# Kernel optimization log

Measured on AMD Instinct MI355X. Metric: run time of the kernel, lower is better.

The kernel has to match this reference:

```python
import jax, jax.numpy as jnp
import numpy as np

HEAD_DIM = 128
NUM_Q_HEADS = 16
NUM_KV_HEADS = 8
EPS = 1e-6


def _rope_tables(seq_len, head_dim, base=10000.0):
    inv_freq = 1.0 / (base ** (np.arange(0, head_dim, 2, dtype=np.float32) / head_dim))
    t = np.arange(seq_len, dtype=np.float32)
    freqs = np.outer(t, inv_freq)                      # [S, hd/2]
    emb = np.concatenate([freqs, freqs], axis=-1)      # [S, hd]
    return jnp.asarray(np.cos(emb)), jnp.asarray(np.sin(emb))


def setup_inputs() -> dict:
    key = jax.random.key(0)
    k1, k2, k3 = jax.random.split(key, 3)
    B, S, D = 2, 2048, 2048
    qo_dim = NUM_Q_HEADS * HEAD_DIM
    kv_dim = NUM_KV_HEADS * HEAD_DIM
    x = jax.random.normal(k1, (B, S, D), dtype=jnp.float32)
    w_qkv = jax.random.normal(k2, (qo_dim + 2 * kv_dim, D), dtype=jnp.float32) * 0.02
    w_o = jax.random.normal(k3, (D, qo_dim), dtype=jnp.float32) * 0.02
    pos_cos, pos_sin = _rope_tables(S, HEAD_DIM)
    return {
        "x": x,
        "pos_cos": pos_cos,
        "pos_sin": pos_sin,
        "w_qkv": w_qkv,
        "w_o": w_o,
        "q_norm_w": jnp.ones((HEAD_DIM,), dtype=jnp.float32),
        "k_norm_w": jnp.ones((HEAD_DIM,), dtype=jnp.float32),
    }


def _rms_norm(h, w):
    # per-head RMSNorm over last dim (head_dim)
    var = jnp.mean(jnp.square(h), axis=-1, keepdims=True)
    return h * jax.lax.rsqrt(var + EPS) * w


def _rotate_half(h):
    h1, h2 = jnp.split(h, 2, axis=-1)
    return jnp.concatenate([-h2, h1], axis=-1)


def _apply_rope(h, cos, sin):
    # h: [B, S, H, hd]; cos/sin: [S, hd]
    c = cos[None, :, None, :]
    s = sin[None, :, None, :]
    return h * c + _rotate_half(h) * s


def reference(x, pos_cos, pos_sin, w_qkv, w_o, q_norm_w, k_norm_w):
    B, S, D = x.shape
    hd = HEAD_DIM
    qkv = jnp.einsum("bsd,ed->bse", x, w_qkv).reshape(B, S, -1, hd)
    q = qkv[:, :, :NUM_Q_HEADS]                                   # [B,S,Hq,hd]
    k = qkv[:, :, NUM_Q_HEADS:NUM_Q_HEADS + NUM_KV_HEADS]         # [B,S,Hk,hd]
    v = qkv[:, :, NUM_Q_HEADS + NUM_KV_HEADS:]                    # [B,S,Hk,hd]

    q = _apply_rope(_rms_norm(q, q_norm_w), pos_cos, pos_sin)
    k = _apply_rope(_rms_norm(k, k_norm_w), pos_cos, pos_sin)

    # GQA: expand kv heads to match query heads
    rep = NUM_Q_HEADS // NUM_KV_HEADS
    k = jnp.repeat(k, rep, axis=2)
    v = jnp.repeat(v, rep, axis=2)

    scale = 1.0 / jnp.sqrt(jnp.float32(hd))
    scores = jnp.einsum("bqhd,bkhd->bhqk", q, k) * scale          # [B,H,S,S]
    causal = jnp.tril(jnp.ones((S, S), dtype=bool))
    scores = jnp.where(causal[None, None], scores, jnp.finfo(scores.dtype).min)
    attn = jax.nn.softmax(scores, axis=-1)
    out = jnp.einsum("bhqk,bkhd->bqhd", attn, v)                  # [B,S,H,hd]
    out = out.reshape(B, S, NUM_Q_HEADS * hd)
    return jnp.einsum("bse,de->bsd", out, w_o)
```

## Files before the change

### kernel.cpp

```cpp
#include <hip/hip_runtime.h>
#include <hip/hip_bf16.h>
#include <stdint.h>

#define HD 128
#define NQH 16
#define NKVH 8
#define SEQ 2048
#define DMODEL 2048
#define BATCH 2

typedef __attribute__((ext_vector_type(8))) short bf16x8;
typedef __attribute__((ext_vector_type(4))) float f32x4;
typedef __attribute__((ext_vector_type(16))) float f32x16;

__device__ __forceinline__ ushort f2bf(float f){
  union { float f; uint32_t u; } v; v.f = f;
  uint32_t u = v.u;
  return (ushort)((u + 0x7FFFu + ((u >> 16) & 1u)) >> 16);
}
__device__ __forceinline__ float bf2f(ushort h){
  union { uint32_t u; float f; } v; v.u = ((uint32_t)h) << 16; return v.f;
}
__device__ __forceinline__ void gload16(const void* g, void* l){
  __builtin_amdgcn_global_load_lds((const __attribute__((address_space(1))) void*)g,
                                   (__attribute__((address_space(3))) void*)l, 16, 0, 0);
}
__device__ __forceinline__ unsigned int cvtpk(float lo, float hi){
  unsigned int r;
  asm("v_cvt_pk_bf16_f32 %0, %1, %2" : "=v"(r) : "v"(lo), "v"(hi));
  return r;
}

__global__ void cvtbf(const float* __restrict__ in, ushort* __restrict__ out, int n4){
  int i = blockIdx.x * 256 + threadIdx.x;
  if (i < n4){
    float4 v = ((const float4*)in)[i];
    ushort4 o;
    o.x = f2bf(v.x); o.y = f2bf(v.y); o.z = f2bf(v.z); o.w = f2bf(v.w);
    ((ushort4*)out)[i] = o;
  }
}

template<int OUTF32>
__global__ __launch_bounds__(256) void gemm_bt(const ushort* __restrict__ A,
                                               const ushort* __restrict__ B,
                                               void* __restrict__ C,
                                               int M, int N, int K){
  __shared__ __align__(16) ushort lA[128*64];
  __shared__ __align__(16) ushort lB[128*64];
  const int tid = threadIdx.x;
  const int l = tid & 63, w = tid >> 6;
  const int m0 = blockIdx.y * 128, n0 = blockIdx.x * 128;
  const int wr = (w >> 1) * 64, wc = (w & 1) * 64;
  f32x4 acc[4][4];
  #pragma unroll
  for (int m=0;m<4;m++)
    #pragma unroll
    for (int n=0;n<4;n++) acc[m][n] = f32x4{0.f,0.f,0.f,0.f};

  const int srow = l >> 3;
  const int scol = ((l & 7) ^ srow) << 3;
  const ushort* gA = A + (size_t)(m0 + w*32 + srow) * K + scol;
  const ushort* gB = B + (size_t)(n0 + w*32 + srow) * K + scol;
  ushort* lAw = &lA[(w*32) * 64];
  ushort* lBw = &lB[(w*32) * 64];

  for (int kt = 0; kt < K; kt += 64){
    __syncthreads();
    #pragma unroll
    for (int j=0;j<4;j++){
      gload16(gA + kt + (size_t)(j*8)*K, lAw + j*8*64);
      gload16(gB + kt + (size_t)(j*8)*K, lBw + j*8*64);
    }
    __syncthreads();
    #pragma unroll
    for (int kk=0; kk<2; kk++){
      bf16x8 af[4], bb[4];
      #pragma unroll
      for (int m=0;m<4;m++){
        int row = wr + m*16 + (l & 15);
        int slot = (kk*4 + (l >> 4)) ^ (row & 7);
        af[m] = *(const bf16x8*)&lA[row*64 + slot*8];
      }
      #pragma unroll
      for (int n=0;n<4;n++){
        int row = wc + n*16 + (l & 15);
        int slot = (kk*4 + (l >> 4)) ^ (row & 7);
        bb[n] = *(const bf16x8*)&lB[row*64 + slot*8];
      }
      #pragma unroll
      for (int m=0;m<4;m++)
        #pragma unroll
        for (int n=0;n<4;n++)
          acc[m][n] = __builtin_amdgcn_mfma_f32_16x16x32_bf16(af[m], bb[n], acc[m][n], 0,0,0);
    }
  }
  #pragma unroll
  for (int m=0;m<4;m++)
    #pragma unroll
    for (int n=0;n<4;n++)
      #pragma unroll
      for (int r=0;r<4;r++){
        size_t row = (size_t)(m0 + wr + m*16 + (l>>4)*4 + r);
        size_t col = (size_t)(n0 + wc + n*16 + (l & 15));
        float v = acc[m][n][r];
        if (OUTF32) ((float*)C)[row*N + col] = v;
        else        ((ushort*)C)[row*N + col] = f2bf(v);
      }
}

__global__ __launch_bounds__(512, 1) void gemm256_bt(const ushort* __restrict__ A,
                                                     const ushort* __restrict__ B,
                                                     ushort* __restrict__ C,
                                                     int M, int N, int K){
  __shared__ __align__(16) ushort lA[2][256*64];
  __shared__ __align__(16) ushort lB[2][256*64];
  const int tid = threadIdx.x;
  const int l = tid & 63, w = tid >> 6;
  const int wm = w >> 2, wn = w & 3;
  const int m0 = blockIdx.y * 256, n0 = blockIdx.x * 256;
  const int NT = K >> 6;

  const int srow = w*8 + (l >> 3);
  const int scol = ((l & 7) ^ (l >> 3)) << 3;

  f32x4 acc[8][4];
  #pragma unroll
  for (int m=0;m<8;m++)
    #pragma unroll
    for (int n=0;n<4;n++) acc[m][n] = f32x4{0.f,0.f,0.f,0.f};

  auto stgA = [&](int t, int h){
    const int bi = t & 1;
    #pragma unroll
    for (int j=0;j<2;j++)
      gload16(A + (size_t)(m0 + h*128 + j*64 + srow)*K + t*64 + scol,
              &lA[bi][(h*128 + j*64 + w*8)*64]);
  };
  auto stgB = [&](int t, int h){
    const int bi = t & 1;
    #pragma unroll
    for (int j=0;j<2;j++)
      gload16(B + (size_t)(n0 + h*128 + j*64 + srow)*K + t*64 + scol,
              &lB[bi][(h*128 + j*64 + w*8)*64]);
  };

  stgA(0,0); stgA(0,1); stgB(0,0); stgB(0,1);
  stgA(1,0); stgB(1,0); stgB(1,1);
  asm volatile("s_waitcnt vmcnt(6)" ::: "memory");
  __builtin_amdgcn_s_barrier();

  for (int t=0; t<NT; t++){
    const int bi = t & 1;
    bf16x8 bfr[4][2];
    #pragma unroll
    for (int q=0; q<4; q++){
      bf16x8 af[2][2];
      #pragma unroll
      for (int mi2=0; mi2<2; mi2++)
        #pragma unroll
        for (int ks=0; ks<2; ks++){
          int row = wm*128 + (q*2 + mi2)*16 + (l & 15);
          int slot = (ks*4 + (l >> 4)) ^ (l & 7);
          af[mi2][ks] = *(const bf16x8*)&lA[bi][row*64 + slot*8];
        }
      if (q == 0){
        #pragma unroll
        for (int ni=0; ni<4; ni++)
          #pragma unroll
          for (int ks=0; ks<2; ks++){
            int row = wn*64 + ni*16 + (l & 15);
            int slot = (ks*4 + (l >> 4)) ^ (l & 7);
            bfr[ni][ks] = *(const bf16x8*)&lB[bi][row*64 + slot*8];
          }
      }
      if (q == 0 && t+1 < NT) stgA(t+1, 1);
      if (q == 1 && t+2 < NT) stgB(t+2, 0);
      if (q == 2 && t+2 < NT) stgB(t+2, 1);
      __builtin_amdgcn_s_barrier();
      asm volatile("s_waitcnt lgkmcnt(0)" ::: "memory");
      if (q == 3 && t+2 < NT) stgA(t+2, 0);
      __builtin_amdgcn_s_setprio(1);
      #pragma unroll
      for (int mi2=0; mi2<2; mi2++)
        #pragma unroll
        for (int ni=0; ni<4; ni++)
          #pragma unroll
          for (int ks=0; ks<2; ks++)
            acc[q*2+mi2][ni] = __builtin_amdgcn_mfma_f32_16x16x32_bf16(
                af[mi2][ks], bfr[ni][ks], acc[q*2+mi2][ni], 0,0,0);
      __builtin_amdgcn_s_setprio(0);
      if (q == 3){
        if (t < NT-2) { asm volatile("s_waitcnt vmcnt(6)" ::: "memory"); }
        else          { asm volatile("s_waitcnt vmcnt(0)" ::: "memory"); }
      }
      __builtin_amdgcn_s_barrier();
    }
  }

  #pragma unroll
  for (int mi=0; mi<8; mi++)
    #pragma unroll
    for (int ni=0; ni<4; ni++)
      #pragma unroll
      for (int r=0; r<4; r++){
        size_t row = (size_t)(m0 + wm*128 + mi*16 + (l>>4)*4 + r);
        size_t col = (size_t)(n0 + wn*64 + ni*16 + (l & 15));
        C[row*N + col] = f2bf(acc[mi][ni][r]);
      }
}

__global__ __launch_bounds__(256) void norm_rope(const ushort* __restrict__ qkv,
                                                 const float* __restrict__ cosT,
                                                 const float* __restrict__ sinT,
                                                 const float* __restrict__ qw,
                                                 const float* __restrict__ kw,
                                                 ushort* __restrict__ Qo,
                                                 ushort* __restrict__ Ko){
  int gw = (blockIdx.x * 256 + threadIdx.x) >> 6;
  int l = threadIdx.x & 63;
  int head = gw % 24;
  int bs = gw / 24;
  int s = bs & (SEQ-1);
  int b = bs >> 11;
  ushort2 hv = *(const ushort2*)(qkv + (size_t)bs*(2*DMODEL) + head*HD + l*2);
  float h0 = bf2f(hv.x), h1 = bf2f(hv.y);
  float ss = h0*h0 + h1*h1;
  #pragma unroll
  for (int m=1; m<64; m<<=1) ss += __shfl_xor(ss, m);
  float rinv = rsqrtf(ss * (1.0f/128.0f) + 1e-6f);
  const float* wp = (head < NQH) ? qw : kw;
  float w0 = wp[l*2], w1 = wp[l*2+1];
  float n0 = h0 * rinv * w0, n1 = h1 * rinv * w1;
  float p0 = __shfl_xor(n0, 32), p1 = __shfl_xor(n1, 32);
  float r0 = (l < 32) ? -p0 : p0;
  float r1 = (l < 32) ? -p1 : p1;
  float c0 = cosT[s*HD + l*2], c1 = cosT[s*HD + l*2 + 1];
  float s0 = sinT[s*HD + l*2], s1 = sinT[s*HD + l*2 + 1];
  float sc = (head < NQH) ? 0.12751656062f : 1.0f;
  ushort2 o;
  o.x = f2bf((n0*c0 + r0*s0) * sc);
  o.y = f2bf((n1*c1 + r1*s1) * sc);
  if (head < NQH)
    *(ushort2*)(Qo + ((size_t)((b*NQH + head)*SEQ) + s)*HD + l*2) = o;
  else
    *(ushort2*)(Ko + ((size_t)((b*NKVH + (head-NQH))*SEQ) + s)*HD + l*2) = o;
}

__global__ __launch_bounds__(256) void vtrans(const ushort* __restrict__ qkv, ushort* __restrict__ vt){
  __shared__ __align__(16) ushort t[64][136];
  int bid = blockIdx.x;
  int st = bid & 31, kh = (bid >> 5) & 7, b = bid >> 8;
  int s0 = st * 64;
  int tid = threadIdx.x;
  #pragma unroll
  for (int it=0; it<4; it++){
    int row = (tid >> 4) + it*16;
    int c = tid & 15;
    uint4 v = *(const uint4*)&qkv[((size_t)(b*SEQ + s0 + row))*(2*DMODEL) + (NQH+NKVH+kh)*HD + c*8];
    *(uint4*)&t[row][c*8] = v;
  }
  __syncthreads();
  #pragma unroll
  for (int it=0; it<4; it++){
    int g = it*256 + tid;
    int d = g >> 3, c = g & 7;
    ushort tmp[8] __attribute__((aligned(16)));
    #pragma unroll
    for (int j=0;j<8;j++) tmp[j] = t[c*8+j][d];
    *(uint4*)&vt[((size_t)((b*NKVH+kh)*HD + d))*SEQ + s0 + c*8] = *(uint4*)tmp;
  }
}

__global__ __launch_bounds__(256, 2) void attn_fwd(const ushort* __restrict__ Q,
                                                   const ushort* __restrict__ Kb,
                                                   const ushort* __restrict__ Vt,
                                                   ushort* __restrict__ O){
  __shared__ __align__(16) ushort lK[2][64*128];
  __shared__ __align__(16) ushort lV[2][128*64];
  const int l = threadIdx.x & 63, w = threadIdx.x >> 6;
  const int wq = w >> 1, wkv = w & 1;
  const int hl = l >> 5, q32 = l & 31;
  const int e = blockIdx.x, head = blockIdx.y, b = blockIdx.z;
  const int kh = head >> 1;

  const ushort* kg = Kb + (size_t)((b*NKVH + kh)*SEQ) * HD;
  const ushort* vg = Vt + (size_t)((b*NKVH + kh)*HD) * SEQ;

  auto STAGE = [&](int t, int bi){
    const int kv0 = t*64;
    #pragma unroll
    for (int j=0;j<4;j++){
      int krow = kv0 + w*16 + j*4 + (l>>4);
      gload16(kg + (size_t)krow*HD + (((l&15) ^ (krow&15))<<3),
              &lK[bi][(w*16 + j*4)*128]);
      int vrow = w*32 + j*8 + (l>>3);
      gload16(vg + (size_t)vrow*SEQ + kv0 + (((l&7) ^ (l>>3))<<3),
              &lV[bi][(w*32 + j*8)*64]);
    }
  };

  auto run_tile = [&](int qt){
    const int qb = qt*64 + wq*32;
    const ushort* qp = Q + ((size_t)((b*NQH + head)*SEQ) + qb + q32) * HD + hl*8;
    bf16x8 qf[8];
    #pragma unroll
    for (int ks=0; ks<8; ks++) qf[ks] = *(const bf16x8*)(qp + ks*16);

    float mrun = -1e30f, lrun = 0.f;
    f32x16 acc[4];
    #pragma unroll
    for (int dt=0;dt<4;dt++)
      #pragma unroll
      for (int r=0;r<16;r++) acc[dt][r] = 0.f;

    STAGE(0, 0);
    __syncthreads();

    for (int t=0; t<=qt; t++){
      if (t < qt) STAGE(t+1, (t+1)&1);
      const int bi = t & 1;
      const bool skip = (t==qt) && (wq==0) && (wkv==1);
      if (!skip){
        f32x16 s;
        #pragma unroll
        for (int r=0;r<16;r++) s[r] = 0.f;
        const int rowT = wkv*32 + q32;
        #pragma unroll
        for (int ks=0; ks<8; ks++){
          int slot = (ks*2 + hl) ^ (rowT & 15);
          bf16x8 kf = *(const bf16x8*)&lK[bi][rowT*128 + slot*8];
          s = __builtin_amdgcn_mfma_f32_32x32x16_bf16(kf, qf[ks], s, 0,0,0);
        }
        if (t==qt && wq==wkv){
          const int qg = qb + q32;
          #pragma unroll
          for (int r=0;r<16;r++){
            int kvg = t*64 + wkv*32 + (r&3) + 8*(r>>2) + 4*hl;
            s[r] = (kvg > qg) ? -1e30f : s[r];
          }
        }
        float t0 = fmaxf(fmaxf(s[0],s[1]),fmaxf(s[2],s[3]));
        float t1 = fmaxf(fmaxf(s[4],s[5]),fmaxf(s[6],s[7]));
        float t2 = fmaxf(fmaxf(s[8],s[9]),fmaxf(s[10],s[11]));
        float t3 = fmaxf(fmaxf(s[12],s[13]),fmaxf(s[14],s[15]));
        float tmax = fmaxf(fmaxf(t0,t1),fmaxf(t2,t3));
        tmax = fmaxf(tmax, __shfl_xor(tmax, 32));
        if (!__all(tmax <= mrun)){
          float mnew = fmaxf(mrun, tmax);
          float corr = __builtin_amdgcn_exp2f(mrun - mnew);
          mrun = mnew; lrun *= corr;
          #pragma unroll
          for (int r=0;r<16;r++){
            int qr = (r&3) + 8*(r>>2) + 4*hl;
            float cr = __shfl(corr, qr);
            acc[0][r]*=cr; acc[1][r]*=cr; acc[2][r]*=cr; acc[3][r]*=cr;
          }
        }
        #pragma unroll
        for (int r=0;r<16;r++) s[r] = __builtin_amdgcn_exp2f(s[r] - mrun);
        float r0s = (s[0]+s[1])+(s[2]+s[3]);
        float r1s = (s[4]+s[5])+(s[6]+s[7]);
        float r2s = (s[8]+s[9])+(s[10]+s[11]);
        float r3s = (s[12]+s[13])+(s[14]+s[15]);
        float rs = (r0s+r1s)+(r2s+r3s);
        rs += __shfl_xor(rs, 32);
        lrun += rs;
        #pragma unroll
        for (int ks2=0; ks2<2; ks2++){
          unsigned int A = cvtpk(s[8*ks2+0], s[8*ks2+1]);
          unsigned int B = cvtpk(s[8*ks2+2], s[8*ks2+3]);
          unsigned int C = cvtpk(s[8*ks2+4], s[8*ks2+5]);
          unsigned int D = cvtpk(s[8*ks2+6], s[8*ks2+7]);
          auto sw0 = __builtin_amdgcn_permlane32_swap(A, C, false, false);
          auto sw1 = __builtin_amdgcn_permlane32_swap(B, D, false, false);
          union { unsigned int u[4]; bf16x8 v; } pw;
          pw.u[0]=sw0[0]; pw.u[1]=sw1[0]; pw.u[2]=sw0[1]; pw.u[3]=sw1[1];
          #pragma unroll
          for (int dt=0; dt<4; dt++){
            int d = dt*32 + q32;
            int slot = (wkv*4 + ks2*2 + hl) ^ (d & 7);
            bf16x8 vf = *(const bf16x8*)&lV[bi][d*64 + slot*8];
            acc[dt] = __builtin_amdgcn_mfma_f32_32x32x16_bf16(pw.v, vf, acc[dt], 0,0,0);
          }
        }
      }
      __syncthreads();
    }

    float* mergeO = (float*)(&lK[0][0]) + wq*4096;
    float* mergeML = (float*)(&lV[0][0]);
    if (wkv == 1){
      #pragma unroll
      for (int dt=0; dt<4; dt++)
        #pragma unroll
        for (int rg=0; rg<4; rg++){
          f32x4 o = { acc[dt][rg*4+0], acc[dt][rg*4+1], acc[dt][rg*4+2], acc[dt][rg*4+3] };
          *(f32x4*)&mergeO[(dt*4+rg)*256 + l*4] = o;
        }
      if (l < 32){
        mergeML[wq*64 + l] = mrun;
        mergeML[wq*64 + 32 + l] = lrun;
      }
    }
    __syncthreads();
    if (wkv == 0){
      float m1 = mergeML[wq*64 + q32];
      float l1 = mergeML[wq*64 + 32 + q32];
      float mf = fmaxf(mrun, m1);
      float c0 = __builtin_amdgcn_exp2f(mrun - mf);
      float c1 = __builtin_amdgcn_exp2f(m1 - mf);
      float lt = lrun*c0 + l1*c1;
      float linv = 1.0f / lt;
      float f0 = c0 * linv, f1 = c1 * linv;
      float g0a[16], g1a[16];
      #pragma unroll
      for (int r=0;r<16;r++){
        int qr = (r&3) + 8*(r>>2) + 4*hl;
        g0a[r] = __shfl(f0, qr);
        g1a[r] = __shfl(f1, qr);
      }
      #pragma unroll
      for (int dt=0; dt<4; dt++)
        #pragma unroll
        for (int rg=0; rg<4; rg++){
          f32x4 o1 = *(const f32x4*)&mergeO[(dt*4+rg)*256 + l*4];
          #pragma unroll
          for (int j=0;j<4;j++){
            int r = rg*4 + j;
            int qr = (r&3) + 8*(r>>2) + 4*hl;
            float val = acc[dt][r]*g0a[r] + o1[j]*g1a[r];
            int orow = qt*64 + wq*32 + qr;
            O[((size_t)(b*SEQ) + orow)*DMODEL + head*HD + dt*32 + q32] = f2bf(val);
          }
        }
    }
    __syncthreads();
  };

  run_tile(e);
  run_tile(31 - e);
}

extern "C" void kernel_launch(void* const* d_in, const int* in_sizes, int n_in,
                              void* d_out, int out_size, void* d_ws, size_t ws_size,
                              hipStream_t stream){
  const float* x    = (const float*)d_in[0];
  const float* pcos = (const float*)d_in[1];
  const float* psin = (const float*)d_in[2];
  const float* wqkv = (const float*)d_in[3];
  const float* wo   = (const float*)d_in[4];
  const float* qnw  = (const float*)d_in[5];
  const float* knw  = (const float*)d_in[6];
  char* ws = (char*)d_ws;

  ushort* xb    = (ushort*)(ws + 0);
  ushort* wqkvb = (ushort*)(ws + 16777216);
  ushort* wob   = (ushort*)(ws + 33554432);
  ushort* qkv   = (ushort*)(ws + 41943040);
  ushort* qbuf  = (ushort*)(ws + 75497472);
  ushort* kbuf  = (ushort*)(ws + 92274688);
  ushort* vtb   = (ushort*)(ws + 100663296);
  ushort* aout  = (ushort*)(ws + 0);

  cvtbf<<<8192, 256, 0, stream>>>(x,    xb,    2097152);
  cvtbf<<<8192, 256, 0, stream>>>(wqkv, wqkvb, 2097152);
  cvtbf<<<4096, 256, 0, stream>>>(wo,   wob,   1048576);

  gemm256_bt<<<dim3(16,16), 512, 0, stream>>>(xb, wqkvb, qkv, 4096, 4096, 2048);

  norm_rope<<<24576, 256, 0, stream>>>(qkv, pcos, psin, qnw, knw, qbuf, kbuf);
  vtrans<<<512, 256, 0, stream>>>(qkv, vtb);

  attn_fwd<<<dim3(16,16,2), 256, 0, stream>>>(qbuf, kbuf, vtb, aout);

  gemm_bt<1><<<dim3(16,32), 256, 0, stream>>>(aout, wob, d_out, 4096, 2048, 2048);
}
```

Measured before the change: 224.1 us.

## Restructure attention: one q-tile per block, single V buffer, finer-grained waits

Each attention block now handles a single query tile, launched longest-first across a 1D grid of 1024 blocks. Previously each block processed a paired short and long tile to balance causal work. The V LDS buffer drops from double to single buffering so three blocks can share a CU. K for the next tile and V for the current tile are issued together, and explicit vmcnt waits let QK^T and softmax overlap the V load. MFMA phases are bracketed with s_setprio, and more barriers are added per iteration, which may cost some synchronisation overhead.

```diff
diff --git a/kernel.cpp b/kernel.cpp
--- a/kernel.cpp
+++ b/kernel.cpp
@@ -272,174 +272,192 @@
   }
 }
 
-__global__ __launch_bounds__(256, 2) void attn_fwd(const ushort* __restrict__ Q,
+__global__ __launch_bounds__(256, 3) void attn_fwd(const ushort* __restrict__ Q,
                                                    const ushort* __restrict__ Kb,
                                                    const ushort* __restrict__ Vt,
                                                    ushort* __restrict__ O){
   __shared__ __align__(16) ushort lK[2][64*128];
-  __shared__ __align__(16) ushort lV[2][128*64];
+  __shared__ __align__(16) ushort lV[128*64];
   const int l = threadIdx.x & 63, w = threadIdx.x >> 6;
   const int wq = w >> 1, wkv = w & 1;
   const int hl = l >> 5, q32 = l & 31;
-  const int e = blockIdx.x, head = blockIdx.y, b = blockIdx.z;
+  const int bid = blockIdx.x;
+  const int qt = 31 - (bid >> 5);
+  const int bh = bid & 31;
+  const int head = bh & 15, b = bh >> 4;
   const int kh = head >> 1;
 
   const ushort* kg = Kb + (size_t)((b*NKVH + kh)*SEQ) * HD;
   const ushort* vg = Vt + (size_t)((b*NKVH + kh)*HD) * SEQ;
 
-  auto STAGE = [&](int t, int bi){
+  auto STAGE_K = [&](int t, int bi){
     const int kv0 = t*64;
     #pragma unroll
     for (int j=0;j<4;j++){
       int krow = kv0 + w*16 + j*4 + (l>>4);
       gload16(kg + (size_t)krow*HD + (((l&15) ^ (krow&15))<<3),
               &lK[bi][(w*16 + j*4)*128]);
+    }
+  };
+  auto STAGE_V = [&](int t){
+    const int kv0 = t*64;
+    #pragma unroll
+    for (int j=0;j<4;j++){
       int vrow = w*32 + j*8 + (l>>3);
       gload16(vg + (size_t)vrow*SEQ + kv0 + (((l&7) ^ (l>>3))<<3),
-              &lV[bi][(w*32 + j*8)*64]);
+              &lV[(w*32 + j*8)*64]);
     }
   };
 
-  auto run_tile = [&](int qt){
-    const int qb = qt*64 + wq*32;
-    const ushort* qp = Q + ((size_t)((b*NQH + head)*SEQ) + qb + q32) * HD + hl*8;
-    bf16x8 qf[8];
-    #pragma unroll
-    for (int ks=0; ks<8; ks++) qf[ks] = *(const bf16x8*)(qp + ks*16);
-
-    float mrun = -1e30f, lrun = 0.f;
-    f32x16 acc[4];
-    #pragma unroll
-    for (int dt=0;dt<4;dt++)
-      #pragma unroll
-      for (int r=0;r<16;r++) acc[dt][r] = 0.f;
-
-    STAGE(0, 0);
-    __syncthreads();
-
-    for (int t=0; t<=qt; t++){
-      if (t < qt) STAGE(t+1, (t+1)&1);
-      const int bi = t & 1;
-      const bool skip = (t==qt) && (wq==0) && (wkv==1);
-      if (!skip){
-        f32x16 s;
-        #pragma unroll
-        for (int r=0;r<16;r++) s[r] = 0.f;
-        const int rowT = wkv*32 + q32;
-        #pragma unroll
-        for (int ks=0; ks<8; ks++){
-          int slot = (ks*2 + hl) ^ (rowT & 15);
-          bf16x8 kf = *(const bf16x8*)&lK[bi][rowT*128 + slot*8];
-          s = __builtin_amdgcn_mfma_f32_32x32x16_bf16(kf, qf[ks], s, 0,0,0);
+  const int qb = qt*64 + wq*32;
+  const ushort* qp = Q + ((size_t)((b*NQH + head)*SEQ) + qb + q32) * HD + hl*8;
+  bf16x8 qf[8];
+  #pragma unroll
+  for (int ks=0; ks<8; ks++) qf[ks] = *(const bf16x8*)(qp + ks*16);
+
+  float mrun = -1e30f, lrun = 0.f;
+  f32x16 acc[4];
+  #pragma unroll
+  for (int dt=0;dt<4;dt++)
+    #pragma unroll
+    for (int r=0;r<16;r++) acc[dt][r] = 0.f;
+
+  STAGE_K(0, 0);
+
+  for (int t=0; t<=qt; t++){
+    const int bi = t & 1;
+    STAGE_V(t);
+    STAGE_K(t < qt ? t+1 : qt, bi^1);
+    asm volatile("s_waitcnt vmcnt(8)" ::: "memory");
+    __builtin_amdgcn_s_barrier();
+
+    const bool skip = (t==qt) && (wq==0) && (wkv==1);
+    f32x16 s;
+    if (!skip){
+      #pragma unroll
+      for (int r=0;r<16;r++) s[r] = 0.f;
+      const int rowT = wkv*32 + q32;
+      __builtin_amdgcn_s_setprio(1);
+      #pragma unroll
+      for (int ks=0; ks<8; ks++){
+        int slot = (ks*2 + hl) ^ (rowT & 15);
+        bf16x8 kf = *(const bf16x8*)&lK[bi][rowT*128 + slot*8];
+        s = __builtin_amdgcn_mfma_f32_32x32x16_bf16(kf, qf[ks], s, 0,0,0);
+      }
+      __builtin_amdgcn_s_setprio(0);
+      if (t==qt && wq==wkv){
+        const int qg = qb + q32;
+        #pragma unroll
+        for (int r=0;r<16;r++){
+          int kvg = t*64 + wkv*32 + (r&3) + 8*(r>>2) + 4*hl;
+          s[r] = (kvg > qg) ? -1e30f : s[r];
         }
-        if (t==qt && wq==wkv){
-          const int qg = qb + q32;
-          #pragma unroll
-          for (int r=0;r<16;r++){
-            int kvg = t*64 + wkv*32 + (r&3) + 8*(r>>2) + 4*hl;
-            s[r] = (kvg > qg) ? -1e30f : s[r];
-          }
+      }
+      float t0 = fmaxf(fmaxf(s[0],s[1]),fmaxf(s[2],s[3]));
+      float t1 = fmaxf(fmaxf(s[4],s[5]),fmaxf(s[6],s[7]));
+      float t2 = fmaxf(fmaxf(s[8],s[9]),fmaxf(s[10],s[11]));
+      float t3 = fmaxf(fmaxf(s[12],s[13]),fmaxf(s[14],s[15]));
+      float tmax = fmaxf(fmaxf(t0,t1),fmaxf(t2,t3));
+      tmax = fmaxf(tmax, __shfl_xor(tmax, 32));
+      if (!__all(tmax <= mrun)){
+        float mnew = fmaxf(mrun, tmax);
+        float corr = __builtin_amdgcn_exp2f(mrun - mnew);
+        mrun = mnew; lrun *= corr;
+        #pragma unroll
+        for (int r=0;r<16;r++){
+          int qr = (r&3) + 8*(r>>2) + 4*hl;
+          float cr = __shfl(corr, qr);
+          acc[0][r]*=cr; acc[1][r]*=cr; acc[2][r]*=cr; acc[3][r]*=cr;
         }
-        float t0 = fmaxf(fmaxf(s[0],s[1]),fmaxf(s[2],s[3]));
-        float t1 = fmaxf(fmaxf(s[4],s[5]),fmaxf(s[6],s[7]));
-        float t2 = fmaxf(fmaxf(s[8],s[9]),fmaxf(s[10],s[11]));
-        float t3 = fmaxf(fmaxf(s[12],s[13]),fmaxf(s[14],s[15]));
-        float tmax = fmaxf(fmaxf(t0,t1),fmaxf(t2,t3));
-        tmax = fmaxf(tmax, __shfl_xor(tmax, 32));
-        if (!__all(tmax <= mrun)){
-          float mnew = fmaxf(mrun, tmax);
-          float corr = __builtin_amdgcn_exp2f(mrun - mnew);
-          mrun = mnew; lrun *= corr;
-          #pragma unroll
-          for (int r=0;r<16;r++){
-            int qr = (r&3) + 8*(r>>2) + 4*hl;
-            float cr = __shfl(corr, qr);
-            acc[0][r]*=cr; acc[1][r]*=cr; acc[2][r]*=cr; acc[3][r]*=cr;
-          }
+      }
+      #pragma unroll
+      for (int r=0;r<16;r++) s[r] = __builtin_amdgcn_exp2f(s[r] - mrun);
+      float r0s = (s[0]+s[1])+(s[2]+s[3]);
+      float r1s = (s[4]+s[5])+(s[6]+s[7]);
+      float r2s = (s[8]+s[9])+(s[10]+s[11]);
+      float r3s = (s[12]+s[13])+(s[14]+s[15]);
+      float rs = (r0s+r1s)+(r2s+r3s);
+      rs += __shfl_xor(rs, 32);
+      lrun += rs;
+    }
+    asm volatile("s_waitcnt vmcnt(4)" ::: "memory");
+    __builtin_amdgcn_s_barrier();
+    if (!skip){
+      __builtin_amdgcn_s_setprio(1);
+      #pragma unroll
+      for (int ks2=0; ks2<2; ks2++){
+        unsigned int A = cvtpk(s[8*ks2+0], s[8*ks2+1]);
+        unsigned int B = cvtpk(s[8*ks2+2], s[8*ks2+3]);
+        unsigned int C = cvtpk(s[8*ks2+4], s[8*ks2+5]);
+        unsigned int D = cvtpk(s[8*ks2+6], s[8*ks2+7]);
+        auto sw0 = __builtin_amdgcn_permlane32_swap(A, C, false, false);
+        auto sw1 = __builtin_amdgcn_permlane32_swap(B, D, false, false);
+        union { unsigned int u[4]; bf16x8 v; } pw;
+        pw.u[0]=sw0[0]; pw.u[1]=sw1[0]; pw.u[2]=sw0[1]; pw.u[3]=sw1[1];
+        #pragma unroll
+        for (int dt=0; dt<4; dt++){
+          int d = dt*32 + q32;
+          int slot = (wkv*4 + ks2*2 + hl) ^ (d & 7);
+          bf16x8 vf = *(const bf16x8*)&lV[d*64 + slot*8];
+          acc[dt] = __builtin_amdgcn_mfma_f32_32x32x16_bf16(pw.v, vf, acc[dt], 0,0,0);
         }
-        #pragma unroll
-        for (int r=0;r<16;r++) s[r] = __builtin_amdgcn_exp2f(s[r] - mrun);
-        float r0s = (s[0]+s[1])+(s[2]+s[3]);
-        float r1s = (s[4]+s[5])+(s[6]+s[7]);
-        float r2s = (s[8]+s[9])+(s[10]+s[11]);
-        float r3s = (s[12]+s[13])+(s[14]+s[15]);
-        float rs = (r0s+r1s)+(r2s+r3s);
-        rs += __shfl_xor(rs, 32);
-        lrun += rs;
-        #pragma unroll
-        for (int ks2=0; ks2<2; ks2++){
-          unsigned int A = cvtpk(s[8*ks2+0], s[8*ks2+1]);
-          unsigned int B = cvtpk(s[8*ks2+2], s[8*ks2+3]);
-          unsigned int C = cvtpk(s[8*ks2+4], s[8*ks2+5]);
-          unsigned int D = cvtpk(s[8*ks2+6], s[8*ks2+7]);
-          auto sw0 = __builtin_amdgcn_permlane32_swap(A, C, false, false);
-          auto sw1 = __builtin_amdgcn_permlane32_swap(B, D, false, false);
-          union { unsigned int u[4]; bf16x8 v; } pw;
-          pw.u[0]=sw0[0]; pw.u[1]=sw1[0]; pw.u[2]=sw0[1]; pw.u[3]=sw1[1];
-          #pragma unroll
-          for (int dt=0; dt<4; dt++){
-            int d = dt*32 + q32;
-            int slot = (wkv*4 + ks2*2 + hl) ^ (d & 7);
-            bf16x8 vf = *(const bf16x8*)&lV[bi][d*64 + slot*8];
-            acc[dt] = __builtin_amdgcn_mfma_f32_32x32x16_bf16(pw.v, vf, acc[dt], 0,0,0);
-          }
+      }
+      __builtin_amdgcn_s_setprio(0);
+    }
+    asm volatile("s_waitcnt lgkmcnt(0)" ::: "memory");
+    __builtin_amdgcn_s_barrier();
+  }
+
+  asm volatile("s_waitcnt vmcnt(0)" ::: "memory");
+  __builtin_amdgcn_s_barrier();
+
+  float* mergeO = (float*)(&lK[0][0]) + wq*4096;
+  float* mergeML = (float*)(&lV[0]);
+  if (wkv == 1){
+    #pragma unroll
+    for (int dt=0; dt<4; dt++)
+      #pragma unroll
+      for (int rg=0; rg<4; rg++){
+        f32x4 o = { acc[dt][rg*4+0], acc[dt][rg*4+1], acc[dt][rg*4+2], acc[dt][rg*4+3] };
+        *(f32x4*)&mergeO[(dt*4+rg)*256 + l*4] = o;
+      }
+    if (l < 32){
+      mergeML[wq*64 + l] = mrun;
+      mergeML[wq*64 + 32 + l] = lrun;
+    }
+  }
+  __syncthreads();
+  if (wkv == 0){
+    float m1 = mergeML[wq*64 + q32];
+    float l1 = mergeML[wq*64 + 32 + q32];
+    float mf = fmaxf(mrun, m1);
+    float c0 = __builtin_amdgcn_exp2f(mrun - mf);
+    float c1 = __builtin_amdgcn_exp2f(m1 - mf);
+    float lt = lrun*c0 + l1*c1;
+    float linv = 1.0f / lt;
+    float f0 = c0 * linv, f1 = c1 * linv;
+    float g0a[16], g1a[16];
+    #pragma unroll
+    for (int r=0;r<16;r++){
+      int qr = (r&3) + 8*(r>>2) + 4*hl;
+      g0a[r] = __shfl(f0, qr);
+      g1a[r] = __shfl(f1, qr);
+    }
+    #pragma unroll
+    for (int dt=0; dt<4; dt++)
+      #pragma unroll
+      for (int rg=0; rg<4; rg++){
+        f32x4 o1 = *(const f32x4*)&mergeO[(dt*4+rg)*256 + l*4];
+        #pragma unroll
+        for (int j=0;j<4;j++){
+          int r = rg*4 + j;
+          int qr = (r&3) + 8*(r>>2) + 4*hl;
+          float val = acc[dt][r]*g0a[r] + o1[j]*g1a[r];
+          int orow = qt*64 + wq*32 + qr;
+          O[((size_t)(b*SEQ) + orow)*DMODEL + head*HD + dt*32 + q32] = f2bf(val);
         }
       }
-      __syncthreads();
-    }
-
-    float* mergeO = (float*)(&lK[0][0]) + wq*4096;
-    float* mergeML = (float*)(&lV[0][0]);
-    if (wkv == 1){
-      #pragma unroll
-      for (int dt=0; dt<4; dt++)
-        #pragma unroll
-        for (int rg=0; rg<4; rg++){
-          f32x4 o = { acc[dt][rg*4+0], acc[dt][rg*4+1], acc[dt][rg*4+2], acc[dt][rg*4+3] };
-          *(f32x4*)&mergeO[(dt*4+rg)*256 + l*4] = o;
-        }
-      if (l < 32){
-        mergeML[wq*64 + l] = mrun;
-        mergeML[wq*64 + 32 + l] = lrun;
-      }
-    }
-    __syncthreads();
-    if (wkv == 0){
-      float m1 = mergeML[wq*64 + q32];
-      float l1 = mergeML[wq*64 + 32 + q32];
-      float mf = fmaxf(mrun, m1);
-      float c0 = __builtin_amdgcn_exp2f(mrun - mf);
-      float c1 = __builtin_amdgcn_exp2f(m1 - mf);
-      float lt = lrun*c0 + l1*c1;
-      float linv = 1.0f / lt;
-      float f0 = c0 * linv, f1 = c1 * linv;
-      float g0a[16], g1a[16];
-      #pragma unroll
-      for (int r=0;r<16;r++){
-        int qr = (r&3) + 8*(r>>2) + 4*hl;
-        g0a[r] = __shfl(f0, qr);
-        g1a[r] = __shfl(f1, qr);
-      }
-      #pragma unroll
-      for (int dt=0; dt<4; dt++)
-        #pragma unroll
-        for (int rg=0; rg<4; rg++){
-          f32x4 o1 = *(const f32x4*)&mergeO[(dt*4+rg)*256 + l*4];
-          #pragma unroll
-          for (int j=0;j<4;j++){
-            int r = rg*4 + j;
-            int qr = (r&3) + 8*(r>>2) + 4*hl;
-            float val = acc[dt][r]*g0a[r] + o1[j]*g1a[r];
-            int orow = qt*64 + wq*32 + qr;
-            O[((size_t)(b*SEQ) + orow)*DMODEL + head*HD + dt*32 + q32] = f2bf(val);
-          }
-        }
-    }
-    __syncthreads();
-  };
-
-  run_tile(e);
-  run_tile(31 - e);
+  }
 }
 
 extern "C" void kernel_launch(void* const* d_in, const int* in_sizes, int n_in,
@@ -472,7 +490,7 @@
   norm_rope<<<24576, 256, 0, stream>>>(qkv, pcos, psin, qnw, knw, qbuf, kbuf);
   vtrans<<<512, 256, 0, stream>>>(qkv, vtb);
 
-  attn_fwd<<<dim3(16,16,2), 256, 0, stream>>>(qbuf, kbuf, vtb, aout);
+  attn_fwd<<<dim3(1024), 256, 0, stream>>>(qbuf, kbuf, vtb, aout);
 
   gemm_bt<1><<<dim3(16,32), 256, 0, stream>>>(aout, wob, d_out, 4096, 2048, 2048);
 }
```

After: 228.2 us. Within noise of the previous version (+1.8%).

## Replace output projection GEMM with pipelined 256x128 double-buffered kernel

Applied to the files above, without the earlier changes.

Swaps the simple 128x128 single-buffered output-projection GEMM for a 512-thread 256x128 tile kernel. It double-buffers LDS with async global-to-LDS loads staged across sub-iterations and raises MFMA priority. The aim is to hide load latency and improve data reuse per block. It uses more LDS and registers per block, so occupancy drops to one block per CU.

```diff
diff --git a/kernel.cpp b/kernel.cpp
--- a/kernel.cpp
+++ b/kernel.cpp
@@ -39,74 +39,6 @@
     o.x = f2bf(v.x); o.y = f2bf(v.y); o.z = f2bf(v.z); o.w = f2bf(v.w);
     ((ushort4*)out)[i] = o;
   }
-}
-
-template<int OUTF32>
-__global__ __launch_bounds__(256) void gemm_bt(const ushort* __restrict__ A,
-                                               const ushort* __restrict__ B,
-                                               void* __restrict__ C,
-                                               int M, int N, int K){
-  __shared__ __align__(16) ushort lA[128*64];
-  __shared__ __align__(16) ushort lB[128*64];
-  const int tid = threadIdx.x;
-  const int l = tid & 63, w = tid >> 6;
-  const int m0 = blockIdx.y * 128, n0 = blockIdx.x * 128;
-  const int wr = (w >> 1) * 64, wc = (w & 1) * 64;
-  f32x4 acc[4][4];
-  #pragma unroll
-  for (int m=0;m<4;m++)
-    #pragma unroll
-    for (int n=0;n<4;n++) acc[m][n] = f32x4{0.f,0.f,0.f,0.f};
-
-  const int srow = l >> 3;
-  const int scol = ((l & 7) ^ srow) << 3;
-  const ushort* gA = A + (size_t)(m0 + w*32 + srow) * K + scol;
-  const ushort* gB = B + (size_t)(n0 + w*32 + srow) * K + scol;
-  ushort* lAw = &lA[(w*32) * 64];
-  ushort* lBw = &lB[(w*32) * 64];
-
-  for (int kt = 0; kt < K; kt += 64){
-    __syncthreads();
-    #pragma unroll
-    for (int j=0;j<4;j++){
-      gload16(gA + kt + (size_t)(j*8)*K, lAw + j*8*64);
-      gload16(gB + kt + (size_t)(j*8)*K, lBw + j*8*64);
-    }
-    __syncthreads();
-    #pragma unroll
-    for (int kk=0; kk<2; kk++){
-      bf16x8 af[4], bb[4];
-      #pragma unroll
-      for (int m=0;m<4;m++){
-        int row = wr + m*16 + (l & 15);
-        int slot = (kk*4 + (l >> 4)) ^ (row & 7);
-        af[m] = *(const bf16x8*)&lA[row*64 + slot*8];
-      }
-      #pragma unroll
-      for (int n=0;n<4;n++){
-        int row = wc + n*16 + (l & 15);
-        int slot = (kk*4 + (l >> 4)) ^ (row & 7);
-        bb[n] = *(const bf16x8*)&lB[row*64 + slot*8];
-      }
-      #pragma unroll
-      for (int m=0;m<4;m++)
-        #pragma unroll
-        for (int n=0;n<4;n++)
-          acc[m][n] = __builtin_amdgcn_mfma_f32_16x16x32_bf16(af[m], bb[n], acc[m][n], 0,0,0);
-    }
-  }
-  #pragma unroll
-  for (int m=0;m<4;m++)
-    #pragma unroll
-    for (int n=0;n<4;n++)
-      #pragma unroll
-      for (int r=0;r<4;r++){
-        size_t row = (size_t)(m0 + wr + m*16 + (l>>4)*4 + r);
-        size_t col = (size_t)(n0 + wc + n*16 + (l & 15));
-        float v = acc[m][n][r];
-        if (OUTF32) ((float*)C)[row*N + col] = v;
-        else        ((ushort*)C)[row*N + col] = f2bf(v);
-      }
 }
 
 __global__ __launch_bounds__(512, 1) void gemm256_bt(const ushort* __restrict__ A,
@@ -207,6 +139,106 @@
         size_t row = (size_t)(m0 + wm*128 + mi*16 + (l>>4)*4 + r);
         size_t col = (size_t)(n0 + wn*64 + ni*16 + (l & 15));
         C[row*N + col] = f2bf(acc[mi][ni][r]);
+      }
+}
+
+__global__ __launch_bounds__(512, 1) void gemm256x128_bt(const ushort* __restrict__ A,
+                                                         const ushort* __restrict__ B,
+                                                         float* __restrict__ C,
+                                                         int M, int N, int K){
+  __shared__ __align__(16) ushort lA[2][256*64];
+  __shared__ __align__(16) ushort lB[2][128*64];
+  const int tid = threadIdx.x;
+  const int l = tid & 63, w = tid >> 6;
+  const int wm = w >> 2, wn = w & 3;
+  const int m0 = blockIdx.y * 256, n0 = blockIdx.x * 128;
+  const int NT = K >> 6;
+
+  const int srow = w*8 + (l >> 3);
+  const int scol = ((l & 7) ^ (l >> 3)) << 3;
+
+  f32x4 acc[8][2];
+  #pragma unroll
+  for (int m=0;m<8;m++)
+    #pragma unroll
+    for (int n=0;n<2;n++) acc[m][n] = f32x4{0.f,0.f,0.f,0.f};
+
+  auto stgA = [&](int t, int h){
+    const int bi = t & 1;
+    #pragma unroll
+    for (int j=0;j<2;j++)
+      gload16(A + (size_t)(m0 + h*128 + j*64 + srow)*K + t*64 + scol,
+              &lA[bi][(h*128 + j*64 + w*8)*64]);
+  };
+  auto stgB = [&](int t){
+    const int bi = t & 1;
+    #pragma unroll
+    for (int j=0;j<2;j++)
+      gload16(B + (size_t)(n0 + j*64 + srow)*K + t*64 + scol,
+              &lB[bi][(j*64 + w*8)*64]);
+  };
+
+  stgA(0,0); stgA(0,1); stgB(0);
+  stgB(1); stgA(1,0);
+  asm volatile("s_waitcnt vmcnt(4)" ::: "memory");
+  __builtin_amdgcn_s_barrier();
+
+  for (int t=0; t<NT; t++){
+    const int bi = t & 1;
+    bf16x8 bfr[2][2];
+    #pragma unroll
+    for (int q=0; q<4; q++){
+      bf16x8 af[2][2];
+      #pragma unroll
+      for (int mi2=0; mi2<2; mi2++)
+        #pragma unroll
+        for (int ks=0; ks<2; ks++){
+          int row = wm*128 + (q*2 + mi2)*16 + (l & 15);
+          int slot = (ks*4 + (l >> 4)) ^ (l & 7);
+          af[mi2][ks] = *(const bf16x8*)&lA[bi][row*64 + slot*8];
+        }
+      if (q == 0){
+        #pragma unroll
+        for (int ni=0; ni<2; ni++)
+          #pragma unroll
+          for (int ks=0; ks<2; ks++){
+            int row = wn*32 + ni*16 + (l & 15);
+            int slot = (ks*4 + (l >> 4)) ^ (l & 7);
+            bfr[ni][ks] = *(const bf16x8*)&lB[bi][row*64 + slot*8];
+          }
+      }
+      if (q == 0 && t+1 < NT) stgA(t+1, 1);
+      if (q == 2 && t+2 < NT) stgB(t+2);
+      __builtin_amdgcn_s_barrier();
+      asm volatile("s_waitcnt lgkmcnt(0)" ::: "memory");
+      if (q == 3 && t+2 < NT) stgA(t+2, 0);
+      __builtin_amdgcn_s_setprio(1);
+      #pragma unroll
+      for (int mi2=0; mi2<2; mi2++)
+        #pragma unroll
+        for (int ni=0; ni<2; ni++)
+          #pragma unroll
+          for (int ks=0; ks<2; ks++)
+            acc[q*2+mi2][ni] = __builtin_amdgcn_mfma_f32_16x16x32_bf16(
+                af[mi2][ks], bfr[ni][ks], acc[q*2+mi2][ni], 0,0,0);
+      __builtin_amdgcn_s_setprio(0);
+      if (q == 3){
+        if (t < NT-2) { asm volatile("s_waitcnt vmcnt(4)" ::: "memory"); }
+        else          { asm volatile("s_waitcnt vmcnt(0)" ::: "memory"); }
+      }
+      __builtin_amdgcn_s_barrier();
+    }
+  }
+
+  #pragma unroll
+  for (int mi=0; mi<8; mi++)
+    #pragma unroll
+    for (int ni=0; ni<2; ni++)
+      #pragma unroll
+      for (int r=0; r<4; r++){
+        size_t row = (size_t)(m0 + wm*128 + mi*16 + (l>>4)*4 + r);
+        size_t col = (size_t)(n0 + wn*32 + ni*16 + (l & 15));
+        C[row*N + col] = acc[mi][ni][r];
       }
 }
 
@@ -474,5 +506,5 @@
 
   attn_fwd<<<dim3(16,16,2), 256, 0, stream>>>(qbuf, kbuf, vtb, aout);
 
-  gemm_bt<1><<<dim3(16,32), 256, 0, stream>>>(aout, wob, d_out, 4096, 2048, 2048);
-}
+  gemm256x128_bt<<<dim3(16,16), 512, 0, stream>>>(aout, wob, (float*)d_out, 4096, 2048, 2048);
+}
```

Result: slower. 234.4 us (+4.6%).
